# Kernel tuning notes

Measured on AMD Instinct MI355X. Metric: run time of the kernel, lower is better.

Reference implementation:

```python
import jax, jax.numpy as jnp
import numpy as np

N = 50000      # nodes
E = 800000     # edges (no self loops; reference appends one self loop per node implicitly)
D = 128        # input_dim
NUM_MSGS = 21
OUT = 63


def setup_inputs() -> dict:
    key = jax.random.key(0)
    ks = jax.random.split(key, 12)
    x = jax.random.normal(ks[0], (N, 1, D), dtype=jnp.float32)
    # edge_index with src != dst (remove_self_loops is then a no-op, faithful to torch module)
    src = jax.random.randint(ks[1], (E,), 0, N)
    off = jax.random.randint(ks[2], (E,), 1, N)
    dst = (src + off) % N
    edge_index = jnp.stack([src, dst]).astype(jnp.int64)
    batch = jnp.zeros((N,), dtype=jnp.int64)  # unused by forward
    s = 0.05
    W_msg = jax.random.normal(ks[3], (NUM_MSGS, D, D), dtype=jnp.float32) * s
    b_msg = jax.random.normal(ks[4], (NUM_MSGS, D), dtype=jnp.float32) * s
    W_upd = jax.random.normal(ks[5], (NUM_MSGS, D, 2 * D), dtype=jnp.float32) * s
    W1 = jax.random.normal(ks[6], (256, D), dtype=jnp.float32) * s
    b1 = jax.random.normal(ks[7], (256,), dtype=jnp.float32) * s
    W2 = jax.random.normal(ks[8], (128, 256), dtype=jnp.float32) * s
    b2 = jax.random.normal(ks[9], (128,), dtype=jnp.float32) * s
    W3 = jax.random.normal(ks[10], (OUT, 128), dtype=jnp.float32) * s
    b3 = jax.random.normal(ks[11], (OUT,), dtype=jnp.float32) * s
    return {"x": x, "edge_index": edge_index, "batch": batch,
            "W_msg": W_msg, "b_msg": b_msg, "W_upd": W_upd,
            "W1": W1, "b1": b1, "W2": W2, "b2": b2, "W3": W3, "b3": b3}


def reference(x, edge_index, batch, W_msg, b_msg, W_upd, W1, b1, W2, b2, W3, b3):
    x = x[:, 0, :]  # squeeze(1) -> [N, D]
    src, dst = edge_index[0], edge_index[1]

    def layer(h, p):
        Wm, bm, Wu = p
        # message is per-source-node: transform once per node, then gather
        m = jnp.tanh(h @ Wm.T + bm)                              # [N, D]
        # aggr='add' over edges + one self loop per node (add_self_loops)
        aggr = jax.ops.segment_sum(m[src], dst, num_segments=N) + m
        z = jnp.concatenate([aggr, h], axis=-1) @ Wu.T           # [N, D]
        return jax.nn.relu(z), None  # update ReLU; outer ReLU is idempotent

    h, _ = jax.lax.scan(layer, x, (W_msg, b_msg, W_upd))
    h = jax.nn.relu(h @ W1.T + b1)
    h = jax.nn.relu(h @ W2.T + b2)
    return h @ W3.T + b3  # [N, 63]
```

## Files before the change

### kernel.cpp

```cpp
#include <hip/hip_runtime.h>
#include <cstdint>

#define NN 50000
#define NE 800000

typedef __attribute__((ext_vector_type(8))) short    s16x8;
typedef __attribute__((ext_vector_type(4))) float    f32x4;
typedef __attribute__((ext_vector_type(8))) float    f32x8;
typedef __attribute__((ext_vector_type(4))) unsigned short u16x4;
typedef _Float16 f16x8 __attribute__((ext_vector_type(8)));

typedef unsigned short ushort_t;
typedef unsigned int   uint_t;

__device__ __forceinline__ unsigned short f2h(float v){
    _Float16 f = (_Float16)v; unsigned short u; __builtin_memcpy(&u, &f, 2); return u;
}
__device__ __forceinline__ float h2f(unsigned short u){
    _Float16 f; __builtin_memcpy(&f, &u, 2); return (float)f;
}

__global__ void hist_kernel(const int* __restrict__ dst, int* counts){
    int e = blockIdx.x * blockDim.x + threadIdx.x;
    if (e < NE) atomicAdd(&counts[dst[e]], 1);
}

__global__ void blocksum_kernel(const int* __restrict__ counts, int* __restrict__ bsum){
    __shared__ int sd[256];
    int i = blockIdx.x * 256 + threadIdx.x;
    int c = (i < NN) ? counts[i] : 0;
    sd[threadIdx.x] = c; __syncthreads();
    for (int o = 128; o > 0; o >>= 1){
        if (threadIdx.x < o) sd[threadIdx.x] += sd[threadIdx.x + o];
        __syncthreads();
    }
    if (threadIdx.x == 0) bsum[blockIdx.x] = sd[0];
}

__global__ void scanb_kernel(const int* __restrict__ bsum, int* __restrict__ boff,
                             int* __restrict__ row_start, int nb){
    __shared__ int sd[256];
    int t = threadIdx.x;
    int v = (t < nb) ? bsum[t] : 0;
    sd[t] = v; __syncthreads();
    for (int o = 1; o < 256; o <<= 1){
        int u = (t >= o) ? sd[t - o] : 0;
        __syncthreads();
        sd[t] += u;
        __syncthreads();
    }
    if (t < nb) boff[t] = sd[t] - v;
    if (t == 0) row_start[NN] = NE;
}

__global__ void localscan_kernel(const int* __restrict__ counts, const int* __restrict__ boff,
                                 int* __restrict__ row_start, int* __restrict__ cursor){
    __shared__ int sd[256];
    int t = threadIdx.x, i = blockIdx.x * 256 + t;
    int c = (i < NN) ? counts[i] : 0;
    sd[t] = c; __syncthreads();
    for (int o = 1; o < 256; o <<= 1){
        int u = (t >= o) ? sd[t - o] : 0;
        __syncthreads();
        sd[t] += u;
        __syncthreads();
    }
    if (i < NN){
        int ex = boff[blockIdx.x] + sd[t] - c;
        row_start[i] = ex; cursor[i] = ex;
    }
}

__global__ void scatter_kernel(const int* __restrict__ src, const int* __restrict__ dst,
                               int* cursor, int* __restrict__ colv){
    int e = blockIdx.x * blockDim.x + threadIdx.x;
    if (e < NE){
        int pos = atomicAdd(&cursor[dst[e]], 1);
        colv[pos] = src[e];
    }
}

__global__ void convert_x_kernel(const float* __restrict__ x, ushort_t* __restrict__ xf){
    int i = blockIdx.x * blockDim.x + threadIdx.x;
    if (i >= NN * 32) return;
    f32x4 v = *reinterpret_cast<const f32x4*>(x + (size_t)i * 4);
    u16x4 h;
#pragma unroll
    for (int j = 0; j < 4; ++j) h[j] = f2h(v[j]);
    *reinterpret_cast<u16x4*>(xf + (size_t)i * 4) = h;
}

__global__ void prep_wmsg(const float* __restrict__ W, ushort_t* __restrict__ hi,
                          ushort_t* __restrict__ lo){
    int idx = blockIdx.x * blockDim.x + threadIdx.x;
    const int per = 4 * 8 * 512;
    if (idx >= 21 * per) return;
    int layer = idx / per, r = idx % per;
    int kk = r / 4096, nt = (r / 512) & 7, lane = (r / 8) & 63, i = r & 7;
    int c = nt * 16 + (lane & 15);
    int k = kk * 32 + (lane >> 4) * 8 + i;
    float w = W[(size_t)layer * 16384 + c * 128 + k];
    unsigned short h = f2h(w);
    hi[idx] = h; lo[idx] = f2h(w - h2f(h));
}

__global__ void prep_wupd(const float* __restrict__ W, ushort_t* __restrict__ hi,
                          ushort_t* __restrict__ lo){
    int idx = blockIdx.x * blockDim.x + threadIdx.x;
    const int per = 8 * 8 * 512;
    if (idx >= 21 * per) return;
    int layer = idx / per, r = idx % per;
    int kk = r / 4096, nt = (r / 512) & 7, lane = (r / 8) & 63, i = r & 7;
    int c = nt * 16 + (lane & 15);
    int k = kk * 32 + (lane >> 4) * 8 + i;
    float w = W[(size_t)layer * 32768 + c * 256 + k];
    unsigned short h = f2h(w);
    hi[idx] = h; lo[idx] = f2h(w - h2f(h));
}

__global__ void prep_mlp(const float* __restrict__ W1, const float* __restrict__ W2,
                         const float* __restrict__ W3,
                         ushort_t* w1h, ushort_t* w1l,
                         ushort_t* w2h, ushort_t* w2l,
                         ushort_t* w3h, ushort_t* w3l){
    int idx = blockIdx.x * blockDim.x + threadIdx.x;
    if (idx >= 73728) return;
    const float* W; ushort_t *ph, *pl; int NT, Kld, nc, local;
    if (idx < 32768)      { local = idx;         W = W1; ph = w1h; pl = w1l; NT = 16; Kld = 128; nc = 256; }
    else if (idx < 65536) { local = idx - 32768; W = W2; ph = w2h; pl = w2l; NT = 8;  Kld = 256; nc = 128; }
    else                  { local = idx - 65536; W = W3; ph = w3h; pl = w3l; NT = 4;  Kld = 128; nc = 63;  }
    int i = local & 7, lane = (local >> 3) & 63, nt = (local >> 9) % NT, kk = local / (512 * NT);
    int c = nt * 16 + (lane & 15);
    int k = kk * 32 + (lane >> 4) * 8 + i;
    float w = (c < nc) ? W[c * Kld + k] : 0.f;
    unsigned short h = f2h(w);
    ph[local] = h; pl[local] = f2h(w - h2f(h));
}

template<int KK1, int KK2, int NT>
__device__ __forceinline__ void core_f16(
    const ushort_t* __restrict__ A1, const ushort_t* __restrict__ A2,
    const ushort_t* __restrict__ Bh, const ushort_t* __restrict__ Bl,
    int NTtot, int nt0, int waveRow0, int lane, f32x4 (&acc)[NT])
{
    const int lm = lane & 15;
    const int lk = (lane >> 4) * 8;
#pragma unroll
    for (int kk = 0; kk < KK1 + KK2; ++kk){
        const ushort_t* ap; int ld, kc;
        if (kk < KK1){ ap = A1; ld = KK1 * 32; kc = kk * 32 + lk; }
        else         { ap = A2; ld = KK2 * 32; kc = (kk - KK1) * 32 + lk; }
        f16x8 af = *reinterpret_cast<const f16x8*>(ap + (size_t)(waveRow0 + lm) * ld + kc);
        const ushort_t* bp = Bh + ((size_t)(kk * NTtot + nt0)) * 512 + lane * 8;
        const ushort_t* bq = Bl + ((size_t)(kk * NTtot + nt0)) * 512 + lane * 8;
#pragma unroll
        for (int nt = 0; nt < NT; ++nt){
            f16x8 bh = *reinterpret_cast<const f16x8*>(bp + nt * 512);
            f16x8 bl = *reinterpret_cast<const f16x8*>(bq + nt * 512);
            acc[nt] = __builtin_amdgcn_mfma_f32_16x16x32_f16(af, bh, acc[nt], 0, 0, 0);
            acc[nt] = __builtin_amdgcn_mfma_f32_16x16x32_f16(af, bl, acc[nt], 0, 0, 0);
        }
    }
}

#define LDS_STRIDE 136

template<int NT, int ACT, bool HAS_BIAS>
__device__ __forceinline__ void epi_stage(
    f32x4 (&acc)[NT], const float* __restrict__ bias, int colOffE,
    ushort_t* lds, int w, int lane)
{
    const int lm = lane & 15;
    const int cr = (lane >> 4) * 4;
#pragma unroll
    for (int nt = 0; nt < NT; ++nt){
        float bv = HAS_BIAS ? bias[colOffE + nt * 16 + lm] : 0.f;
#pragma unroll
        for (int j = 0; j < 4; ++j){
            float v = acc[nt][j] + bv;
            if (ACT == 1) v = v > 0.f ? v : 0.f;
            else if (ACT == 2) v = tanhf(v);
            lds[(w * 16 + cr + j) * LDS_STRIDE + nt * 16 + lm] = f2h(v);
        }
    }
}

__device__ __forceinline__ void flush_tile(
    const ushort_t* lds, ushort_t* __restrict__ out,
    int blockRow0, int ldcE, int colOffE, int tid)
{
#pragma unroll
    for (int it = 0; it < 4; ++it){
        int idx  = it * 256 + tid;
        int row  = idx >> 4;
        int colE = (idx & 15) * 8;
        int g = blockRow0 + row;
        if (g < NN)
            *reinterpret_cast<s16x8*>(out + (size_t)g * ldcE + colOffE + colE) =
                *reinterpret_cast<const s16x8*>(lds + row * LDS_STRIDE + colE);
    }
}

template<int KK1, int NT, int ACT, bool HAS_BIAS, int OUTMODE>
__global__ __launch_bounds__(256) void gemm_f16(
    const ushort_t* __restrict__ A1,
    const ushort_t* __restrict__ Bh, const ushort_t* __restrict__ Bl, int NTtot,
    const float* __restrict__ bias,
    ushort_t* __restrict__ Cs, float* __restrict__ Cf, int ldcE, int ncols)
{
    __shared__ ushort_t lds[64 * LDS_STRIDE];
    const int lane = threadIdx.x & 63;
    const int w    = threadIdx.x >> 6;
    const int nt0  = blockIdx.y * NT;
    const int colOffE = blockIdx.y * (NT * 16);
    const int waveRow0 = blockIdx.x * 64 + w * 16;
    f32x4 acc[NT];
#pragma unroll
    for (int nt = 0; nt < NT; ++nt)
#pragma unroll
        for (int j = 0; j < 4; ++j) acc[nt][j] = 0.f;
    core_f16<KK1, 0, NT>(A1, nullptr, Bh, Bl, NTtot, nt0, waveRow0, lane, acc);

    if constexpr (OUTMODE == 2){
        epi_stage<NT, ACT, HAS_BIAS>(acc, bias, colOffE, lds, w, lane);
        __syncthreads();
        flush_tile(lds, Cs, blockIdx.x * 64, ldcE, colOffE, threadIdx.x);
    } else {
        const int lm = lane & 15;
        const int cr = (lane >> 4) * 4;
#pragma unroll
        for (int nt = 0; nt < NT; ++nt){
            int col = colOffE + nt * 16 + lm;
            if (col >= ncols) continue;
            float bv = HAS_BIAS ? bias[col] : 0.f;
#pragma unroll
            for (int j = 0; j < 4; ++j){
                int g = waveRow0 + cr + j;
                if (g < NN){
                    float v = acc[nt][j] + bv;
                    if (ACT == 1) v = v > 0.f ? v : 0.f;
                    else if (ACT == 2) v = tanhf(v);
                    Cf[(size_t)g * ldcE + col] = v;
                }
            }
        }
    }
}

template<bool WITH_MSG>
__global__ __launch_bounds__(256) void fused_update_msg(
    const ushort_t* __restrict__ ag, const ushort_t* __restrict__ h,
    const ushort_t* __restrict__ Wuh, const ushort_t* __restrict__ Wul,
    const ushort_t* __restrict__ Wmh, const ushort_t* __restrict__ Wml,
    const float* __restrict__ bm,
    ushort_t* __restrict__ h_out, ushort_t* __restrict__ m_out)
{
    __shared__ ushort_t lds[64 * LDS_STRIDE];
    const int lane = threadIdx.x & 63;
    const int w    = threadIdx.x >> 6;
    const int waveRow0 = blockIdx.x * 64 + w * 16;
    const int lm = lane & 15;
    const int lk = (lane >> 4) * 8;

    f32x4 acc[8];
#pragma unroll
    for (int nt = 0; nt < 8; ++nt)
#pragma unroll
        for (int j = 0; j < 4; ++j) acc[nt][j] = 0.f;
    core_f16<4, 4, 8>(ag, h, Wuh, Wul, 8, 0, waveRow0, lane, acc);
    epi_stage<8, 1, false>(acc, nullptr, 0, lds, w, lane);
    __syncthreads();
    flush_tile(lds, h_out, blockIdx.x * 64, 128, 0, threadIdx.x);

    if constexpr (WITH_MSG){
        __syncthreads();
        f32x4 acc2[8];
#pragma unroll
        for (int nt = 0; nt < 8; ++nt)
#pragma unroll
            for (int j = 0; j < 4; ++j) acc2[nt][j] = 0.f;
#pragma unroll
        for (int kk = 0; kk < 4; ++kk){
            f16x8 af = *reinterpret_cast<const f16x8*>(lds + (w * 16 + lm) * LDS_STRIDE + kk * 32 + lk);
            const ushort_t* bp = Wmh + (size_t)(kk * 8) * 512 + lane * 8;
            const ushort_t* bq = Wml + (size_t)(kk * 8) * 512 + lane * 8;
#pragma unroll
            for (int nt = 0; nt < 8; ++nt){
                f16x8 bh = *reinterpret_cast<const f16x8*>(bp + nt * 512);
                f16x8 bl = *reinterpret_cast<const f16x8*>(bq + nt * 512);
                acc2[nt] = __builtin_amdgcn_mfma_f32_16x16x32_f16(af, bh, acc2[nt], 0, 0, 0);
                acc2[nt] = __builtin_amdgcn_mfma_f32_16x16x32_f16(af, bl, acc2[nt], 0, 0, 0);
            }
        }
        epi_stage<8, 2, true>(acc2, bm, 0, lds, w, lane);
        __syncthreads();
        flush_tile(lds, m_out, blockIdx.x * 64, 128, 0, threadIdx.x);
    }
}

__global__ __launch_bounds__(256) void aggregate_kernel(
    const ushort_t* __restrict__ m,
    const int* __restrict__ row_start, const int* __restrict__ cols,
    ushort_t* __restrict__ ag)
{
    int wid  = (blockIdx.x * 256 + threadIdx.x) >> 6;
    int lane = threadIdx.x & 63;
    int s0 = row_start[wid], s1 = row_start[wid + 1];
    const uint_t* mp = (const uint_t*)m;
    size_t self = (size_t)wid * 64 + lane;
    uint_t v = mp[self];
    float a0 = h2f((unsigned short)v);
    float a1 = h2f((unsigned short)(v >> 16));
    int e = s0;
    for (; e + 3 < s1; e += 4){
        uint_t v0 = mp[(size_t)cols[e]     * 64 + lane];
        uint_t v1 = mp[(size_t)cols[e + 1] * 64 + lane];
        uint_t v2 = mp[(size_t)cols[e + 2] * 64 + lane];
        uint_t v3 = mp[(size_t)cols[e + 3] * 64 + lane];
        a0 += h2f((unsigned short)v0) + h2f((unsigned short)v1)
            + h2f((unsigned short)v2) + h2f((unsigned short)v3);
        a1 += h2f((unsigned short)(v0 >> 16)) + h2f((unsigned short)(v1 >> 16))
            + h2f((unsigned short)(v2 >> 16)) + h2f((unsigned short)(v3 >> 16));
    }
    for (; e < s1; ++e){
        uint_t v0 = mp[(size_t)cols[e] * 64 + lane];
        a0 += h2f((unsigned short)v0);
        a1 += h2f((unsigned short)(v0 >> 16));
    }
    ((uint_t*)ag)[self] = (uint_t)f2h(a0) | ((uint_t)f2h(a1) << 16);
}

extern "C" void kernel_launch(void* const* d_in, const int* in_sizes, int n_in,
                              void* d_out, int out_size, void* d_ws, size_t ws_size,
                              hipStream_t stream)
{
    const float* x     = (const float*)d_in[0];
    const int*   ei    = (const int*)d_in[1];
    const float* W_msg = (const float*)d_in[3];
    const float* b_msg = (const float*)d_in[4];
    const float* W_upd = (const float*)d_in[5];
    const float* W1    = (const float*)d_in[6];
    const float* b1    = (const float*)d_in[7];
    const float* W2    = (const float*)d_in[8];
    const float* b2    = (const float*)d_in[9];
    const float* W3    = (const float*)d_in[10];
    const float* b3    = (const float*)d_in[11];
    const int* srcp = ei;
    const int* dstp = ei + NE;

    char* ws = (char*)d_ws;
    size_t off = 0;
    auto carve = [&](size_t bytes) -> void* {
        void* p = ws + off;
        off += (bytes + 255) & ~(size_t)255;
        return p;
    };
    const size_t FBUF = (size_t)NN * 128 * 2;
    ushort_t* xf = (ushort_t*)carve(FBUF);
    ushort_t* hA = (ushort_t*)carve(FBUF);
    ushort_t* m  = (ushort_t*)carve(FBUF);
    ushort_t* ag = (ushort_t*)carve(FBUF);

    int* counts    = (int*)carve((size_t)NN * 4);
    int* cursor    = (int*)carve((size_t)NN * 4);
    int* row_start = (int*)carve(((size_t)NN + 1) * 4);
    int* bsum      = (int*)carve(256 * 4);
    int* boff      = (int*)carve(256 * 4);
    int* colv      = (int*)carve((size_t)NE * 4);

    ushort_t* wmsg_hi = (ushort_t*)carve((size_t)21 * 16384 * 2);
    ushort_t* wmsg_lo = (ushort_t*)carve((size_t)21 * 16384 * 2);
    ushort_t* wupd_hi = (ushort_t*)carve((size_t)21 * 32768 * 2);
    ushort_t* wupd_lo = (ushort_t*)carve((size_t)21 * 32768 * 2);
    ushort_t* w1_hi   = (ushort_t*)carve(32768 * 2);
    ushort_t* w1_lo   = (ushort_t*)carve(32768 * 2);
    ushort_t* w2_hi   = (ushort_t*)carve(32768 * 2);
    ushort_t* w2_lo   = (ushort_t*)carve(32768 * 2);
    ushort_t* w3_hi   = (ushort_t*)carve(8192 * 2);
    ushort_t* w3_lo   = (ushort_t*)carve(8192 * 2);
    (void)carve(65536);

    const int NB = (NN + 255) / 256;
    const int GB = (NN + 63) / 64;

    hipMemsetAsync(counts, 0, (size_t)NN * 4, stream);
    hist_kernel<<<(NE + 255) / 256, 256, 0, stream>>>(dstp, counts);
    blocksum_kernel<<<NB, 256, 0, stream>>>(counts, bsum);
    scanb_kernel<<<1, 256, 0, stream>>>(bsum, boff, row_start, NB);
    localscan_kernel<<<NB, 256, 0, stream>>>(counts, boff, row_start, cursor);
    scatter_kernel<<<(NE + 255) / 256, 256, 0, stream>>>(srcp, dstp, cursor, colv);

    convert_x_kernel<<<(NN * 32 + 255) / 256, 256, 0, stream>>>(x, xf);
    prep_wmsg<<<(21 * 16384 + 255) / 256, 256, 0, stream>>>(W_msg, wmsg_hi, wmsg_lo);
    prep_wupd<<<(21 * 32768 + 255) / 256, 256, 0, stream>>>(W_upd, wupd_hi, wupd_lo);
    prep_mlp<<<288, 256, 0, stream>>>(W1, W2, W3, w1_hi, w1_lo, w2_hi, w2_lo, w3_hi, w3_lo);

    gemm_f16<4, 8, 2, true, 2><<<GB, 256, 0, stream>>>(
        xf, wmsg_hi, wmsg_lo, 8, b_msg, m, nullptr, 128, 128);

    const ushort_t* cur = xf;
    ushort_t* nxt = hA;
    for (int l = 0; l < 21; ++l){
        aggregate_kernel<<<NN / 4, 256, 0, stream>>>(m, row_start, colv, ag);
        if (l < 20){
            fused_update_msg<true><<<GB, 256, 0, stream>>>(
                ag, cur,
                wupd_hi + (size_t)l * 32768, wupd_lo + (size_t)l * 32768,
                wmsg_hi + (size_t)(l + 1) * 16384, wmsg_lo + (size_t)(l + 1) * 16384,
                b_msg + (size_t)(l + 1) * 128,
                nxt, m);
        } else {
            fused_update_msg<false><<<GB, 256, 0, stream>>>(
                ag, cur,
                wupd_hi + (size_t)l * 32768, wupd_lo + (size_t)l * 32768,
                nullptr, nullptr, nullptr,
                nxt, nullptr);
        }
        const ushort_t* t = cur; cur = nxt; nxt = (ushort_t*)t;
    }

    ushort_t* h1 = m;
    gemm_f16<4, 8, 1, true, 2><<<dim3(GB, 2), 256, 0, stream>>>(
        cur, w1_hi, w1_lo, 16, b1, h1, nullptr, 256, 256);
    gemm_f16<8, 8, 1, true, 2><<<GB, 256, 0, stream>>>(
        h1, w2_hi, w2_lo, 8, b2, xf, nullptr, 128, 128);
    gemm_f16<4, 4, 0, true, 0><<<GB, 256, 0, stream>>>(
        xf, w3_hi, w3_lo, 4, b3, nullptr, (float*)d_out, 63, 63);
}
```

Measured before the change: 1.664 ms.

## Fuse neighbor aggregation into per-layer update/message kernel with ping-pong message buffers

Each GNN layer previously ran a separate gather-sum aggregate kernel that wrote the aggregated features to global memory, followed by a fused update/message GEMM kernel that read them back. The aggregation now happens inside the layer kernel: each wave gathers 16 rows of neighbor messages into LDS, and the update GEMM reads them from LDS. This removes one launch per layer and the global write/read of the aggregate buffer. Messages are double-buffered (mA/mB) because other blocks still read the old messages while new ones are written. The trade-off is lower occupancy: the GEMM block now carries a latency-bound gather phase, fewer blocks exist (64 rows each), LDS use doubles, and the gather unroll grows from 4 to 8.

```diff
diff --git a/kernel.cpp b/kernel.cpp
--- a/kernel.cpp
+++ b/kernel.cpp
@@ -6,7 +6,6 @@
 
 typedef __attribute__((ext_vector_type(8))) short    s16x8;
 typedef __attribute__((ext_vector_type(4))) float    f32x4;
-typedef __attribute__((ext_vector_type(8))) float    f32x8;
 typedef __attribute__((ext_vector_type(4))) unsigned short u16x4;
 typedef _Float16 f16x8 __attribute__((ext_vector_type(8)));
 
@@ -137,20 +136,17 @@
     ph[local] = h; pl[local] = f2h(w - h2f(h));
 }
 
-template<int KK1, int KK2, int NT>
+template<int KK1, int NT>
 __device__ __forceinline__ void core_f16(
-    const ushort_t* __restrict__ A1, const ushort_t* __restrict__ A2,
+    const ushort_t* __restrict__ A1,
     const ushort_t* __restrict__ Bh, const ushort_t* __restrict__ Bl,
     int NTtot, int nt0, int waveRow0, int lane, f32x4 (&acc)[NT])
 {
     const int lm = lane & 15;
     const int lk = (lane >> 4) * 8;
 #pragma unroll
-    for (int kk = 0; kk < KK1 + KK2; ++kk){
-        const ushort_t* ap; int ld, kc;
-        if (kk < KK1){ ap = A1; ld = KK1 * 32; kc = kk * 32 + lk; }
-        else         { ap = A2; ld = KK2 * 32; kc = (kk - KK1) * 32 + lk; }
-        f16x8 af = *reinterpret_cast<const f16x8*>(ap + (size_t)(waveRow0 + lm) * ld + kc);
+    for (int kk = 0; kk < KK1; ++kk){
+        f16x8 af = *reinterpret_cast<const f16x8*>(A1 + (size_t)(waveRow0 + lm) * (KK1 * 32) + kk * 32 + lk);
         const ushort_t* bp = Bh + ((size_t)(kk * NTtot + nt0)) * 512 + lane * 8;
         const ushort_t* bq = Bl + ((size_t)(kk * NTtot + nt0)) * 512 + lane * 8;
 #pragma unroll
@@ -219,7 +215,7 @@
     for (int nt = 0; nt < NT; ++nt)
 #pragma unroll
         for (int j = 0; j < 4; ++j) acc[nt][j] = 0.f;
-    core_f16<KK1, 0, NT>(A1, nullptr, Bh, Bl, NTtot, nt0, waveRow0, lane, acc);
+    core_f16<KK1, NT>(A1, Bh, Bl, NTtot, nt0, waveRow0, lane, acc);
 
     if constexpr (OUTMODE == 2){
         epi_stage<NT, ACT, HAS_BIAS>(acc, bias, colOffE, lds, w, lane);
@@ -248,32 +244,91 @@
 }
 
 template<bool WITH_MSG>
-__global__ __launch_bounds__(256) void fused_update_msg(
-    const ushort_t* __restrict__ ag, const ushort_t* __restrict__ h,
+__global__ __launch_bounds__(256) void layer_kernel(
+    const ushort_t* __restrict__ m_in, const ushort_t* __restrict__ h,
+    const int* __restrict__ row_start, const int* __restrict__ cols,
     const ushort_t* __restrict__ Wuh, const ushort_t* __restrict__ Wul,
     const ushort_t* __restrict__ Wmh, const ushort_t* __restrict__ Wml,
     const float* __restrict__ bm,
     ushort_t* __restrict__ h_out, ushort_t* __restrict__ m_out)
 {
-    __shared__ ushort_t lds[64 * LDS_STRIDE];
-    const int lane = threadIdx.x & 63;
-    const int w    = threadIdx.x >> 6;
-    const int waveRow0 = blockIdx.x * 64 + w * 16;
+    __shared__ ushort_t lds_ag[64 * LDS_STRIDE];
+    __shared__ ushort_t lds_st[64 * LDS_STRIDE];
+    const int tid  = threadIdx.x;
+    const int lane = tid & 63;
+    const int w    = tid >> 6;
+    const int blockRow0 = blockIdx.x * 64;
     const int lm = lane & 15;
     const int lk = (lane >> 4) * 8;
 
+    const uint_t* mp = (const uint_t*)m_in;
+#pragma unroll 1
+    for (int i = 0; i < 16; ++i){
+        int local = w * 16 + i;
+        int n = blockRow0 + local;
+        float a0 = 0.f, a1 = 0.f;
+        if (n < NN){
+            int s0 = row_start[n], s1 = row_start[n + 1];
+            uint_t v = mp[(size_t)n * 64 + lane];
+            a0 = h2f((ushort_t)v); a1 = h2f((ushort_t)(v >> 16));
+            int e = s0;
+            for (; e + 7 < s1; e += 8){
+                uint_t v0 = mp[(size_t)cols[e]     * 64 + lane];
+                uint_t v1 = mp[(size_t)cols[e + 1] * 64 + lane];
+                uint_t v2 = mp[(size_t)cols[e + 2] * 64 + lane];
+                uint_t v3 = mp[(size_t)cols[e + 3] * 64 + lane];
+                uint_t v4 = mp[(size_t)cols[e + 4] * 64 + lane];
+                uint_t v5 = mp[(size_t)cols[e + 5] * 64 + lane];
+                uint_t v6 = mp[(size_t)cols[e + 6] * 64 + lane];
+                uint_t v7 = mp[(size_t)cols[e + 7] * 64 + lane];
+                a0 += h2f((ushort_t)v0) + h2f((ushort_t)v1) + h2f((ushort_t)v2) + h2f((ushort_t)v3)
+                    + h2f((ushort_t)v4) + h2f((ushort_t)v5) + h2f((ushort_t)v6) + h2f((ushort_t)v7);
+                a1 += h2f((ushort_t)(v0 >> 16)) + h2f((ushort_t)(v1 >> 16)) + h2f((ushort_t)(v2 >> 16)) + h2f((ushort_t)(v3 >> 16))
+                    + h2f((ushort_t)(v4 >> 16)) + h2f((ushort_t)(v5 >> 16)) + h2f((ushort_t)(v6 >> 16)) + h2f((ushort_t)(v7 >> 16));
+            }
+            for (; e + 1 < s1; e += 2){
+                uint_t v0 = mp[(size_t)cols[e]     * 64 + lane];
+                uint_t v1 = mp[(size_t)cols[e + 1] * 64 + lane];
+                a0 += h2f((ushort_t)v0) + h2f((ushort_t)v1);
+                a1 += h2f((ushort_t)(v0 >> 16)) + h2f((ushort_t)(v1 >> 16));
+            }
+            if (e < s1){
+                uint_t v0 = mp[(size_t)cols[e] * 64 + lane];
+                a0 += h2f((ushort_t)v0);
+                a1 += h2f((ushort_t)(v0 >> 16));
+            }
+        }
+        uint_t packed = (uint_t)f2h(a0) | ((uint_t)f2h(a1) << 16);
+        *reinterpret_cast<uint_t*>(&lds_ag[local * LDS_STRIDE + lane * 2]) = packed;
+    }
+
     f32x4 acc[8];
 #pragma unroll
     for (int nt = 0; nt < 8; ++nt)
 #pragma unroll
         for (int j = 0; j < 4; ++j) acc[nt][j] = 0.f;
-    core_f16<4, 4, 8>(ag, h, Wuh, Wul, 8, 0, waveRow0, lane, acc);
-    epi_stage<8, 1, false>(acc, nullptr, 0, lds, w, lane);
+#pragma unroll
+    for (int kk = 0; kk < 8; ++kk){
+        f16x8 af;
+        if (kk < 4)
+            af = *reinterpret_cast<const f16x8*>(&lds_ag[(w * 16 + lm) * LDS_STRIDE + kk * 32 + lk]);
+        else
+            af = *reinterpret_cast<const f16x8*>(h + (size_t)(blockRow0 + w * 16 + lm) * 128 + (kk - 4) * 32 + lk);
+        const ushort_t* bp = Wuh + ((size_t)(kk * 8)) * 512 + lane * 8;
+        const ushort_t* bq = Wul + ((size_t)(kk * 8)) * 512 + lane * 8;
+#pragma unroll
+        for (int nt = 0; nt < 8; ++nt){
+            f16x8 bh = *reinterpret_cast<const f16x8*>(bp + nt * 512);
+            f16x8 bl = *reinterpret_cast<const f16x8*>(bq + nt * 512);
+            acc[nt] = __builtin_amdgcn_mfma_f32_16x16x32_f16(af, bh, acc[nt], 0, 0, 0);
+            acc[nt] = __builtin_amdgcn_mfma_f32_16x16x32_f16(af, bl, acc[nt], 0, 0, 0);
+        }
+    }
+    epi_stage<8, 1, false>(acc, nullptr, 0, lds_st, w, lane);
     __syncthreads();
-    flush_tile(lds, h_out, blockIdx.x * 64, 128, 0, threadIdx.x);
+    flush_tile(lds_st, h_out, blockRow0, 128, 0, tid);
 
     if constexpr (WITH_MSG){
-        __syncthreads();
         f32x4 acc2[8];
 #pragma unroll
         for (int nt = 0; nt < 8; ++nt)
@@ -281,9 +336,9 @@
             for (int j = 0; j < 4; ++j) acc2[nt][j] = 0.f;
 #pragma unroll
         for (int kk = 0; kk < 4; ++kk){
-            f16x8 af = *reinterpret_cast<const f16x8*>(lds + (w * 16 + lm) * LDS_STRIDE + kk * 32 + lk);
-            const ushort_t* bp = Wmh + (size_t)(kk * 8) * 512 + lane * 8;
-            const ushort_t* bq = Wml + (size_t)(kk * 8) * 512 + lane * 8;
+            f16x8 af = *reinterpret_cast<const f16x8*>(&lds_st[(w * 16 + lm) * LDS_STRIDE + kk * 32 + lk]);
+            const ushort_t* bp = Wmh + ((size_t)(kk * 8)) * 512 + lane * 8;
+            const ushort_t* bq = Wml + ((size_t)(kk * 8)) * 512 + lane * 8;
 #pragma unroll
             for (int nt = 0; nt < 8; ++nt){
                 f16x8 bh = *reinterpret_cast<const f16x8*>(bp + nt * 512);
@@ -292,42 +347,11 @@
                 acc2[nt] = __builtin_amdgcn_mfma_f32_16x16x32_f16(af, bl, acc2[nt], 0, 0, 0);
             }
         }
-        epi_stage<8, 2, true>(acc2, bm, 0, lds, w, lane);
-        __syncthreads();
-        flush_tile(lds, m_out, blockIdx.x * 64, 128, 0, threadIdx.x);
-    }
-}
-
-__global__ __launch_bounds__(256) void aggregate_kernel(
-    const ushort_t* __restrict__ m,
-    const int* __restrict__ row_start, const int* __restrict__ cols,
-    ushort_t* __restrict__ ag)
-{
-    int wid  = (blockIdx.x * 256 + threadIdx.x) >> 6;
-    int lane = threadIdx.x & 63;
-    int s0 = row_start[wid], s1 = row_start[wid + 1];
-    const uint_t* mp = (const uint_t*)m;
-    size_t self = (size_t)wid * 64 + lane;
-    uint_t v = mp[self];
-    float a0 = h2f((unsigned short)v);
-    float a1 = h2f((unsigned short)(v >> 16));
-    int e = s0;
-    for (; e + 3 < s1; e += 4){
-        uint_t v0 = mp[(size_t)cols[e]     * 64 + lane];
-        uint_t v1 = mp[(size_t)cols[e + 1] * 64 + lane];
-        uint_t v2 = mp[(size_t)cols[e + 2] * 64 + lane];
-        uint_t v3 = mp[(size_t)cols[e + 3] * 64 + lane];
-        a0 += h2f((unsigned short)v0) + h2f((unsigned short)v1)
-            + h2f((unsigned short)v2) + h2f((unsigned short)v3);
-        a1 += h2f((unsigned short)(v0 >> 16)) + h2f((unsigned short)(v1 >> 16))
-            + h2f((unsigned short)(v2 >> 16)) + h2f((unsigned short)(v3 >> 16));
-    }
-    for (; e < s1; ++e){
-        uint_t v0 = mp[(size_t)cols[e] * 64 + lane];
-        a0 += h2f((unsigned short)v0);
-        a1 += h2f((unsigned short)(v0 >> 16));
-    }
-    ((uint_t*)ag)[self] = (uint_t)f2h(a0) | ((uint_t)f2h(a1) << 16);
+        __syncthreads();
+        epi_stage<8, 2, true>(acc2, bm, 0, lds_st, w, lane);
+        __syncthreads();
+        flush_tile(lds_st, m_out, blockRow0, 128, 0, tid);
+    }
 }
 
 extern "C" void kernel_launch(void* const* d_in, const int* in_sizes, int n_in,
@@ -358,8 +382,8 @@
     const size_t FBUF = (size_t)NN * 128 * 2;
     ushort_t* xf = (ushort_t*)carve(FBUF);
     ushort_t* hA = (ushort_t*)carve(FBUF);
-    ushort_t* m  = (ushort_t*)carve(FBUF);
-    ushort_t* ag = (ushort_t*)carve(FBUF);
+    ushort_t* mA = (ushort_t*)carve(FBUF);
+    ushort_t* mB = (ushort_t*)carve(FBUF);
 
     int* counts    = (int*)carve((size_t)NN * 4);
     int* cursor    = (int*)carve((size_t)NN * 4);
@@ -396,22 +420,23 @@
     prep_mlp<<<288, 256, 0, stream>>>(W1, W2, W3, w1_hi, w1_lo, w2_hi, w2_lo, w3_hi, w3_lo);
 
     gemm_f16<4, 8, 2, true, 2><<<GB, 256, 0, stream>>>(
-        xf, wmsg_hi, wmsg_lo, 8, b_msg, m, nullptr, 128, 128);
+        xf, wmsg_hi, wmsg_lo, 8, b_msg, mA, nullptr, 128, 128);
 
     const ushort_t* cur = xf;
     ushort_t* nxt = hA;
     for (int l = 0; l < 21; ++l){
-        aggregate_kernel<<<NN / 4, 256, 0, stream>>>(m, row_start, colv, ag);
+        const ushort_t* m_in = (l & 1) ? mB : mA;
+        ushort_t*       m_out = (l & 1) ? mA : mB;
         if (l < 20){
-            fused_update_msg<true><<<GB, 256, 0, stream>>>(
-                ag, cur,
+            layer_kernel<true><<<GB, 256, 0, stream>>>(
+                m_in, cur, row_start, colv,
                 wupd_hi + (size_t)l * 32768, wupd_lo + (size_t)l * 32768,
                 wmsg_hi + (size_t)(l + 1) * 16384, wmsg_lo + (size_t)(l + 1) * 16384,
                 b_msg + (size_t)(l + 1) * 128,
-                nxt, m);
+                nxt, m_out);
         } else {
-            fused_update_msg<false><<<GB, 256, 0, stream>>>(
-                ag, cur,
+            layer_kernel<false><<<GB, 256, 0, stream>>>(
+                m_in, cur, row_start, colv,
                 wupd_hi + (size_t)l * 32768, wupd_lo + (size_t)l * 32768,
                 nullptr, nullptr, nullptr,
                 nxt, nullptr);
@@ -419,7 +444,7 @@
         const ushort_t* t = cur; cur = nxt; nxt = (ushort_t*)t;
     }
 
-    ushort_t* h1 = m;
+    ushort_t* h1 = mA;
     gemm_f16<4, 8, 1, true, 2><<<dim3(GB, 2), 256, 0, stream>>>(
         cur, w1_hi, w1_lo, 16, b1, h1, nullptr, 256, 256);
     gemm_f16<8, 8, 1, true, 2><<<GB, 256, 0, stream>>>(
```

Result: slower. 1.812 ms (+8.9%).
